# Optimization experiments

Hardware: AMD Instinct MI355X
Metric: run time of the kernel (lower is better)

## Reference

```python
import jax, jax.numpy as jnp
import numpy as np

DIM = 1024
H = 16
D = DIM // H
SCALE = D ** -0.5
EPS = 1e-5


def _layernorm(x, w, b):
    # force_fp32 LayerNorm over last axis
    xf = x.astype(jnp.float32)
    mu = xf.mean(-1, keepdims=True)
    var = xf.var(-1, keepdims=True)
    y = (xf - mu) / jnp.sqrt(var + EPS) * w.astype(jnp.float32) + b.astype(jnp.float32)
    return y.astype(x.dtype)


def setup_inputs() -> dict:
    key = jax.random.key(0)
    ks = jax.random.split(key, 8)
    x = jax.random.normal(ks[0], (2, 2048, DIM), dtype=jnp.float32)
    qkv_w = jax.random.normal(ks[1], (3 * DIM, DIM), dtype=jnp.float32) * (DIM ** -0.5)
    q_norm_w = jnp.ones((D,), jnp.float32)
    q_norm_b = jnp.zeros((D,), jnp.float32)
    k_norm_w = jnp.ones((D,), jnp.float32)
    k_norm_b = jnp.zeros((D,), jnp.float32)
    proj_w = jax.random.normal(ks[2], (DIM, DIM), dtype=jnp.float32) * (DIM ** -0.5)
    proj_b = jnp.zeros((DIM,), jnp.float32)
    return {"x": x, "qkv_w": qkv_w, "q_norm_w": q_norm_w, "q_norm_b": q_norm_b,
            "k_norm_w": k_norm_w, "k_norm_b": k_norm_b, "proj_w": proj_w, "proj_b": proj_b}


def reference(x, qkv_w, q_norm_w, q_norm_b, k_norm_w, k_norm_b, proj_w, proj_b):
    B, N, C = x.shape
    qkv = x @ qkv_w.T                                  # [B,N,3C]
    qkv = qkv.reshape(B, N, 3, H, D).transpose(2, 0, 3, 1, 4)  # [3,B,H,N,D]
    q, k, v = qkv[0], qkv[1], qkv[2]
    # per-head QK LayerNorm over head_dim
    q = _layernorm(q, q_norm_w, q_norm_b)
    k = _layernorm(k, k_norm_w, k_norm_b)
    # k-centering across sequence
    k = k - k.mean(-2, keepdims=True)
    attn = jnp.einsum('bhnd,bhmd->bhnm', q * SCALE, k)
    attn = attn - attn.max(-1, keepdims=True)
    attn = jax.nn.softmax(attn, axis=-1)
    out = jnp.einsum('bhnm,bhmd->bhnd', attn, v)       # [B,H,N,D]
    out = out.transpose(0, 2, 1, 3).reshape(B, N, C)
    return out @ proj_w.T + proj_b
```

## Files before the change

### kernel.cpp

```cpp
#include <hip/hip_runtime.h>
#include <cstdint>
#include <cstddef>

#define SEQ     2048
#define NBATCH  2
#define CDIM    1024
#define NHEAD   16
#define HDIM    64
#define MTOT    (NBATCH*SEQ)
#define C3      (3*CDIM)
#define LOG2E   1.44269504088896340736f
#define QKSCALE (0.125f*LOG2E)
#define LN_EPS  1e-5f

typedef unsigned short u16;
typedef short s16x8 __attribute__((ext_vector_type(8)));
typedef float f32x4  __attribute__((ext_vector_type(4)));
typedef float f32x16 __attribute__((ext_vector_type(16)));

static __device__ __forceinline__ f32x4 mfma16(s16x8 a, s16x8 b, f32x4 c) {
  return __builtin_amdgcn_mfma_f32_16x16x32_bf16(a, b, c, 0, 0, 0);
}
static __device__ __forceinline__ f32x16 mfma32(s16x8 a, s16x8 b, f32x16 c) {
  return __builtin_amdgcn_mfma_f32_32x32x16_bf16(a, b, c, 0, 0, 0);
}
static __device__ __forceinline__ float b2f(u16 v) {
  return __uint_as_float(((unsigned)v) << 16);
}
static __device__ __forceinline__ u16 f2b(float f) {
  unsigned u = __float_as_uint(f);
  u = u + 0x7fffu + ((u >> 16) & 1u);
  return (u16)(u >> 16);
}
static __device__ __forceinline__ float fexp2(float x) {
  float r;
  asm("v_exp_f32 %0, %1" : "=v"(r) : "v"(x));
  return r;
}

#define G2L16(g, l) __builtin_amdgcn_global_load_lds( \
    (__attribute__((address_space(1))) void*)(g),     \
    (__attribute__((address_space(3))) void*)(l), 16, 0, 0)

__global__ __launch_bounds__(256) void cast_f32_bf16(
    const float* __restrict__ in, u16* __restrict__ out, int n8)
{
  int i = blockIdx.x * 256 + threadIdx.x;
  if (i >= n8) return;
  float4 a = ((const float4*)in)[2*i];
  float4 b = ((const float4*)in)[2*i+1];
  union { u16 u[8]; uint4 v; } r;
  r.u[0]=f2b(a.x); r.u[1]=f2b(a.y); r.u[2]=f2b(a.z); r.u[3]=f2b(a.w);
  r.u[4]=f2b(b.x); r.u[5]=f2b(b.y); r.u[6]=f2b(b.z); r.u[7]=f2b(b.w);
  ((uint4*)out)[i] = r.v;
}

template<bool WRITE_BF16, bool BIAS>
__global__ __launch_bounds__(256) void gemm_nt(
    const u16* __restrict__ A, const u16* __restrict__ Bm,
    void* __restrict__ Cout, const float* __restrict__ bias,
    int M, int Nn, int K)
{
  __shared__ u16 As[128*64];
  __shared__ u16 Bs[128*64];
  const int tid = threadIdx.x;
  const int wave = tid >> 6, lane = tid & 63;
  const int l15 = lane & 15, l4 = lane >> 4;
  const int m0 = blockIdx.y * 128, n0 = blockIdx.x * 128;
  const int wr = (wave >> 1) * 64, wc = (wave & 1) * 64;
  f32x4 acc[4][4] = {};

  for (int k0 = 0; k0 < K; k0 += 64) {
    if (k0) __syncthreads();
#pragma unroll
    for (int i = 0; i < 4; ++i) {
      int ci  = (i*4 + wave)*64 + lane;
      int row = ci >> 3, ch = ci & 7;
      const u16* ga = A  + (size_t)(m0 + row)*K + k0 + ch*8;
      const u16* gb = Bm + (size_t)(n0 + row)*K + k0 + ch*8;
      G2L16(ga, As + (i*4 + wave)*512);
      G2L16(gb, Bs + (i*4 + wave)*512);
    }
    __syncthreads();

#pragma unroll
    for (int kk = 0; kk < 2; ++kk) {
      s16x8 af[4], bf[4];
#pragma unroll
      for (int r = 0; r < 4; ++r)
        af[r] = *(const s16x8*)(As + (wr + r*16 + l15)*64 + kk*32 + l4*8);
#pragma unroll
      for (int c = 0; c < 4; ++c)
        bf[c] = *(const s16x8*)(Bs + (wc + c*16 + l15)*64 + kk*32 + l4*8);
#pragma unroll
      for (int r = 0; r < 4; ++r)
#pragma unroll
        for (int c = 0; c < 4; ++c)
          acc[r][c] = mfma16(af[r], bf[c], acc[r][c]);
    }
  }

#pragma unroll
  for (int r = 0; r < 4; ++r)
#pragma unroll
    for (int c = 0; c < 4; ++c) {
      int row = m0 + wr + r*16 + l4*4;
      int col = n0 + wc + c*16 + l15;
#pragma unroll
      for (int q = 0; q < 4; ++q) {
        float v = acc[r][c][q];
        if (BIAS) v += bias[col];
        if (WRITE_BF16) ((u16*)Cout)[(size_t)(row + q)*Nn + col] = f2b(v);
        else           ((float*)Cout)[(size_t)(row + q)*Nn + col] = v;
      }
    }
}

__global__ __launch_bounds__(256) void ln_qk(
    const u16* __restrict__ qkv,
    const float* __restrict__ qw, const float* __restrict__ qb,
    const float* __restrict__ kw, const float* __restrict__ kb,
    u16* __restrict__ Qs, u16* __restrict__ Kn)
{
  int gw   = blockIdx.x * 4 + (threadIdx.x >> 6);
  int lane = threadIdx.x & 63;
  int m = gw >> 4, h = gw & 15;
  const u16* rowp = qkv + (size_t)m*C3 + h*HDIM + lane;
  int b = m >> 11, n = m & 2047;
  size_t o = ((size_t)(b*NHEAD + h)*SEQ + n)*HDIM + lane;

  float wq = qw[lane], bq = qb[lane], wk = kw[lane], bk = kb[lane];
  float xq = b2f(rowp[0]);
  float xk = b2f(rowp[CDIM]);
  float sq = xq, s2q = xq*xq, sk = xk, s2k = xk*xk;
#pragma unroll
  for (int off = 32; off; off >>= 1) {
    sq += __shfl_xor(sq, off, 64);  s2q += __shfl_xor(s2q, off, 64);
    sk += __shfl_xor(sk, off, 64);  s2k += __shfl_xor(s2k, off, 64);
  }
  float muq = sq*(1.f/64.f), varq = s2q*(1.f/64.f) - muq*muq;
  float muk = sk*(1.f/64.f), vark = s2k*(1.f/64.f) - muk*muk;
  float yq = (xq - muq) * (1.f/sqrtf(varq + LN_EPS)) * wq + bq;
  float yk = (xk - muk) * (1.f/sqrtf(vark + LN_EPS)) * wk + bk;
  Qs[o] = f2b(yq * QKSCALE);
  Kn[o] = f2b(yk);
}

__global__ __launch_bounds__(256) void v_transpose(
    const u16* __restrict__ qkv, u16* __restrict__ Vt)
{
  __shared__ u16 t[64][80];
  int bh = blockIdx.x, j0 = blockIdx.y * 64;
  int b = bh >> 4, h = bh & 15;
  int tid = threadIdx.x;
  int nl = tid >> 2, ch = tid & 3;
  const u16* src = qkv + (size_t)(b*SEQ + j0 + nl)*C3 + 2*CDIM + h*HDIM + ch*16;
  *(uint4*)&t[nl][ch*16]     = *(const uint4*)src;
  *(uint4*)&t[nl][ch*16 + 8] = *(const uint4*)(src + 8);
  __syncthreads();
  int d = tid >> 2, nc = tid & 3;
  u16 o[16];
#pragma unroll
  for (int i = 0; i < 16; ++i) o[i] = t[nc*16 + i][d];
  u16* dst = Vt + ((size_t)(bh*HDIM + d))*SEQ + j0 + nc*16;
  *(uint4*)dst       = *(uint4*)&o[0];
  *(uint4*)(dst + 8) = *(uint4*)&o[8];
}

__global__ __launch_bounds__(256) void flash_attn(
    const u16* __restrict__ Qs, const u16* __restrict__ Kn,
    const u16* __restrict__ Vt, u16* __restrict__ Oa)
{
  __shared__ u16 Kt[2][64*64];
  __shared__ u16 Vs[2][64*64];
  const int tid = threadIdx.x, wave = tid >> 6, lane = tid & 63;
  const int l31 = lane & 31, hi = lane >> 5;
  const int bh = blockIdx.y, q0 = blockIdx.x*128 + wave*32;
  const int sw = l31 & 7;

  const u16* Qrow = Qs + ((size_t)bh*SEQ + q0 + l31)*HDIM + hi*8;
  s16x8 qf[4];
#pragma unroll
  for (int ks = 0; ks < 4; ++ks)
    qf[ks] = *(const s16x8*)(Qrow + ks*16);

  f32x16 o0 = {}, o1 = {};
  float l_run = 0.f;

  const u16* Kg = Kn + (size_t)bh*SEQ*HDIM;
  const u16* Vg = Vt + (size_t)bh*HDIM*SEQ;

  auto STAGE = [&](int jb, int buf) {
#pragma unroll
    for (int i = 0; i < 2; ++i) {
      int ci = (i*4 + wave)*64 + lane;
      int row = ci >> 3, ch = ci & 7;
      int chs = ch ^ (row & 7);
      G2L16(Kg + (size_t)(jb + row)*HDIM + chs*8, Kt[buf] + (i*4 + wave)*512);
      G2L16(Vg + (size_t)row*SEQ + jb + chs*8,    Vs[buf] + (i*4 + wave)*512);
    }
  };

  STAGE(0, 0);
  __syncthreads();

  for (int t = 0; t < SEQ/64; ++t) {
    const int buf = t & 1;
    if (t + 1 < SEQ/64) STAGE((t+1)*64, buf ^ 1);
    const u16* Kb = Kt[buf];
    const u16* Vb = Vs[buf];

    f32x16 s0 = {}, s1 = {};
#pragma unroll
    for (int ks = 0; ks < 4; ++ks) {
      int ch = ((ks*2 + hi) ^ sw) * 8;
      s16x8 k0 = *(const s16x8*)(Kb + l31*64 + ch);
      s16x8 k1 = *(const s16x8*)(Kb + (32 + l31)*64 + ch);
      s0 = mfma32(k0, qf[ks], s0);
      s1 = mfma32(k1, qf[ks], s1);
    }

    float p0[16], p1[16];
#pragma unroll
    for (int i = 0; i < 16; ++i) p0[i] = fexp2(s0[i]);
#pragma unroll
    for (int i = 0; i < 16; ++i) p1[i] = fexp2(s1[i]);
    float s8[8];
#pragma unroll
    for (int i = 0; i < 8; ++i) s8[i] = (p0[i] + p0[i+8]) + (p1[i] + p1[i+8]);
    l_run += ((s8[0]+s8[1]) + (s8[2]+s8[3])) + ((s8[4]+s8[5]) + (s8[6]+s8[7]));

    s16x8 pf[4];
#pragma unroll
    for (int f = 0; f < 2; ++f) {
      const float* pp = f ? p1 : p0;
      unsigned pk[4][2];
#pragma unroll
      for (int q = 0; q < 4; ++q)
#pragma unroll
        for (int i = 0; i < 2; ++i)
          asm("v_cvt_pk_bf16_f32 %0, %1, %2"
              : "=v"(pk[q][i]) : "v"(pp[4*q+2*i]), "v"(pp[4*q+2*i+1]));
#pragma unroll
      for (int kc = 0; kc < 2; ++kc) {
        union { unsigned u[4]; s16x8 v; } bfu;
#pragma unroll
        for (int i = 0; i < 2; ++i) {
          unsigned x = pk[2*kc][i], y = pk[2*kc+1][i];
          asm("v_permlane32_swap_b32 %0, %1" : "+v"(x), "+v"(y));
          bfu.u[i] = x; bfu.u[2+i] = y;
        }
        pf[2*f+kc] = bfu.v;
      }
    }

#pragma unroll
    for (int s = 0; s < 4; ++s) {
      int ch = ((s*2 + hi) ^ sw) * 8;
      s16x8 v0 = *(const s16x8*)(Vb + l31*64 + ch);
      s16x8 v1 = *(const s16x8*)(Vb + (32 + l31)*64 + ch);
      o0 = mfma32(v0, pf[s], o0);
      o1 = mfma32(v1, pf[s], o1);
    }
    __syncthreads();
  }

  float l_all = l_run + __shfl_xor(l_run, 32, 64);
  float inv = 1.f / l_all;
  int b = bh >> 4, h = bh & 15;
  u16* dst = Oa + ((size_t)(b*SEQ + q0 + l31))*CDIM + h*HDIM;
#pragma unroll
  for (int df = 0; df < 2; ++df)
#pragma unroll
    for (int q2 = 0; q2 < 4; ++q2) {
      float a0, a1, a2, a3;
      if (df) { a0=o1[4*q2]; a1=o1[4*q2+1]; a2=o1[4*q2+2]; a3=o1[4*q2+3]; }
      else    { a0=o0[4*q2]; a1=o0[4*q2+1]; a2=o0[4*q2+2]; a3=o0[4*q2+3]; }
      a0 *= inv; a1 *= inv; a2 *= inv; a3 *= inv;
      unsigned w0, w1;
      asm("v_cvt_pk_bf16_f32 %0, %1, %2" : "=v"(w0) : "v"(a0), "v"(a1));
      asm("v_cvt_pk_bf16_f32 %0, %1, %2" : "=v"(w1) : "v"(a2), "v"(a3));
      uint2 st; st.x = w0; st.y = w1;
      *(uint2*)(dst + df*32 + q2*8 + hi*4) = st;
    }
}

extern "C" void kernel_launch(void* const* d_in, const int* in_sizes, int n_in,
                              void* d_out, int out_size, void* d_ws, size_t ws_size,
                              hipStream_t stream)
{
  const float* x      = (const float*)d_in[0];
  const float* qkv_w  = (const float*)d_in[1];
  const float* qnw    = (const float*)d_in[2];
  const float* qnb    = (const float*)d_in[3];
  const float* knw    = (const float*)d_in[4];
  const float* knb    = (const float*)d_in[5];
  const float* proj_w = (const float*)d_in[6];
  const float* proj_b = (const float*)d_in[7];
  float* out = (float*)d_out;

  char* ws = (char*)d_ws;
  u16* xb    = (u16*)(ws);
  u16* wqkv  = (u16*)(ws + (8ull  << 20));
  u16* wproj = (u16*)(ws + (14ull << 20));
  u16* qkvb  = (u16*)(ws + (16ull << 20));
  u16* Qsb   = (u16*)(ws + (40ull << 20));
  u16* Knb   = (u16*)(ws + (48ull << 20));
  u16* Vtb   = (u16*)(ws + (56ull << 20));
  u16* Oab   = (u16*)(ws + (64ull << 20));

  cast_f32_bf16<<<(MTOT*CDIM/8)/256, 256, 0, stream>>>(x, xb, MTOT*CDIM/8);
  cast_f32_bf16<<<(C3*CDIM/8)/256,   256, 0, stream>>>(qkv_w, wqkv, C3*CDIM/8);
  cast_f32_bf16<<<(CDIM*CDIM/8)/256, 256, 0, stream>>>(proj_w, wproj, CDIM*CDIM/8);

  gemm_nt<true, false><<<dim3(C3/128, MTOT/128), 256, 0, stream>>>(
      xb, wqkv, qkvb, nullptr, MTOT, C3, CDIM);

  ln_qk<<<(MTOT*NHEAD)/4, 256, 0, stream>>>(qkvb, qnw, qnb, knw, knb, Qsb, Knb);
  v_transpose<<<dim3(NBATCH*NHEAD, SEQ/64), 256, 0, stream>>>(qkvb, Vtb);

  flash_attn<<<dim3(SEQ/128, NBATCH*NHEAD), 256, 0, stream>>>(Qsb, Knb, Vtb, Oab);

  gemm_nt<false, true><<<dim3(CDIM/128, MTOT/128), 256, 0, stream>>>(
      Oab, wproj, out, proj_b, MTOT, CDIM, CDIM);
}
```

Baseline: 224.7 us.

## Fuse QK layernorm into QKV GEMM epilogue, merge casts, triple-buffer attention

Merges the three cast kernels into one launch and fuses the per-head Q/K LayerNorm into the QKV GEMM epilogue, using cross-lane shuffles over the 16 lanes that hold a head's 64 columns. This removes the ln_qk kernel and its round trip of Q/K through memory. The flash attention loop moves to a 3-stage LDS ring with explicit vmcnt waits, a single barrier per iteration and s_setprio around the MFMA blocks, so loads overlap more with compute. In exchange, LDS use and GEMM epilogue register pressure go up, and the Q/K stores in the epilogue are scattered.

Result: no change. 223.8 us (-0.4%).

```diff
diff --git a/kernel.cpp b/kernel.cpp
--- a/kernel.cpp
+++ b/kernel.cpp
@@ -42,24 +42,35 @@
     (__attribute__((address_space(1))) void*)(g),     \
     (__attribute__((address_space(3))) void*)(l), 16, 0, 0)
 
-__global__ __launch_bounds__(256) void cast_f32_bf16(
-    const float* __restrict__ in, u16* __restrict__ out, int n8)
+#define XSEG   (MTOT*CDIM/8)
+#define W1SEG  (C3*CDIM/8)
+#define W2SEG  (CDIM*CDIM/8)
+__global__ __launch_bounds__(256) void cast_all(
+    const float* __restrict__ x, const float* __restrict__ w1,
+    const float* __restrict__ w2, u16* __restrict__ xb,
+    u16* __restrict__ wqkv, u16* __restrict__ wproj)
 {
   int i = blockIdx.x * 256 + threadIdx.x;
-  if (i >= n8) return;
-  float4 a = ((const float4*)in)[2*i];
-  float4 b = ((const float4*)in)[2*i+1];
+  const float* src; u16* dst; int off;
+  if (i < XSEG)              { src = x;  dst = xb;    off = i; }
+  else if (i < XSEG + W1SEG) { src = w1; dst = wqkv;  off = i - XSEG; }
+  else                       { src = w2; dst = wproj; off = i - XSEG - W1SEG; }
+  float4 a = ((const float4*)src)[2*off];
+  float4 b = ((const float4*)src)[2*off+1];
   union { u16 u[8]; uint4 v; } r;
   r.u[0]=f2b(a.x); r.u[1]=f2b(a.y); r.u[2]=f2b(a.z); r.u[3]=f2b(a.w);
   r.u[4]=f2b(b.x); r.u[5]=f2b(b.y); r.u[6]=f2b(b.z); r.u[7]=f2b(b.w);
-  ((uint4*)out)[i] = r.v;
-}
-
-template<bool WRITE_BF16, bool BIAS>
+  ((uint4*)dst)[off] = r.v;
+}
+
+template<int MODE>
 __global__ __launch_bounds__(256) void gemm_nt(
     const u16* __restrict__ A, const u16* __restrict__ Bm,
     void* __restrict__ Cout, const float* __restrict__ bias,
-    int M, int Nn, int K)
+    int M, int Nn, int K,
+    const float* __restrict__ qw, const float* __restrict__ qb,
+    const float* __restrict__ kw, const float* __restrict__ kb,
+    u16* __restrict__ Qs, u16* __restrict__ Kn)
 {
   __shared__ u16 As[128*64];
   __shared__ u16 Bs[128*64];
@@ -100,50 +111,71 @@
     }
   }
 
-#pragma unroll
-  for (int r = 0; r < 4; ++r)
-#pragma unroll
-    for (int c = 0; c < 4; ++c) {
-      int row = m0 + wr + r*16 + l4*4;
-      int col = n0 + wc + c*16 + l15;
-#pragma unroll
-      for (int q = 0; q < 4; ++q) {
-        float v = acc[r][c][q];
-        if (BIAS) v += bias[col];
-        if (WRITE_BF16) ((u16*)Cout)[(size_t)(row + q)*Nn + col] = f2b(v);
-        else           ((float*)Cout)[(size_t)(row + q)*Nn + col] = v;
+  if (MODE == 0) {
+#pragma unroll
+    for (int r = 0; r < 4; ++r)
+#pragma unroll
+      for (int c = 0; c < 4; ++c) {
+        int row = m0 + wr + r*16 + l4*4;
+        int col = n0 + wc + c*16 + l15;
+#pragma unroll
+        for (int q = 0; q < 4; ++q)
+          ((float*)Cout)[(size_t)(row + q)*Nn + col] = acc[r][c][q] + bias[col];
       }
-    }
-}
-
-__global__ __launch_bounds__(256) void ln_qk(
-    const u16* __restrict__ qkv,
-    const float* __restrict__ qw, const float* __restrict__ qb,
-    const float* __restrict__ kw, const float* __restrict__ kb,
-    u16* __restrict__ Qs, u16* __restrict__ Kn)
-{
-  int gw   = blockIdx.x * 4 + (threadIdx.x >> 6);
-  int lane = threadIdx.x & 63;
-  int m = gw >> 4, h = gw & 15;
-  const u16* rowp = qkv + (size_t)m*C3 + h*HDIM + lane;
-  int b = m >> 11, n = m & 2047;
-  size_t o = ((size_t)(b*NHEAD + h)*SEQ + n)*HDIM + lane;
-
-  float wq = qw[lane], bq = qb[lane], wk = kw[lane], bk = kb[lane];
-  float xq = b2f(rowp[0]);
-  float xk = b2f(rowp[CDIM]);
-  float sq = xq, s2q = xq*xq, sk = xk, s2k = xk*xk;
-#pragma unroll
-  for (int off = 32; off; off >>= 1) {
-    sq += __shfl_xor(sq, off, 64);  s2q += __shfl_xor(s2q, off, 64);
-    sk += __shfl_xor(sk, off, 64);  s2k += __shfl_xor(s2k, off, 64);
+  } else {
+    const int colbase = n0 + wc;
+    if (colbase >= 2*CDIM) {
+#pragma unroll
+      for (int r = 0; r < 4; ++r)
+#pragma unroll
+        for (int c = 0; c < 4; ++c) {
+          int row = m0 + wr + r*16 + l4*4;
+          int col = colbase + c*16 + l15;
+#pragma unroll
+          for (int q = 0; q < 4; ++q)
+            ((u16*)Cout)[(size_t)(row + q)*Nn + col] = f2b(acc[r][c][q]);
+        }
+    } else {
+      const bool isQ = colbase < CDIM;
+      const int cq = isQ ? colbase : colbase - CDIM;
+      const int h  = cq >> 6;
+      const float* wv = isQ ? qw : kw;
+      const float* bv = isQ ? qb : kb;
+      u16* dst = isQ ? Qs : Kn;
+      const float scale = isQ ? QKSCALE : 1.f;
+      float wl[4], bl[4];
+#pragma unroll
+      for (int c = 0; c < 4; ++c) { wl[c] = wv[c*16 + l15]; bl[c] = bv[c*16 + l15]; }
+#pragma unroll
+      for (int r = 0; r < 4; ++r) {
+        float mu[4], rs[4];
+#pragma unroll
+        for (int q = 0; q < 4; ++q) {
+          float s = acc[r][0][q] + acc[r][1][q] + acc[r][2][q] + acc[r][3][q];
+          float s2 = acc[r][0][q]*acc[r][0][q] + acc[r][1][q]*acc[r][1][q]
+                   + acc[r][2][q]*acc[r][2][q] + acc[r][3][q]*acc[r][3][q];
+#pragma unroll
+          for (int off = 1; off < 16; off <<= 1) {
+            s  += __shfl_xor(s,  off, 64);
+            s2 += __shfl_xor(s2, off, 64);
+          }
+          float m_ = s * (1.f/64.f);
+          mu[q] = m_;
+          rs[q] = rsqrtf(s2 * (1.f/64.f) - m_*m_ + LN_EPS);
+        }
+#pragma unroll
+        for (int c = 0; c < 4; ++c)
+#pragma unroll
+          for (int q = 0; q < 4; ++q) {
+            int mrow = m0 + wr + r*16 + l4*4 + q;
+            int b = mrow >> 11, ns = mrow & 2047;
+            float y = (acc[r][c][q] - mu[q]) * rs[q] * wl[c] + bl[c];
+            dst[((size_t)(b*NHEAD + h)*SEQ + ns)*HDIM + c*16 + l15] =
+                f2b(y * scale);
+          }
+      }
+    }
   }
-  float muq = sq*(1.f/64.f), varq = s2q*(1.f/64.f) - muq*muq;
-  float muk = sk*(1.f/64.f), vark = s2k*(1.f/64.f) - muk*muk;
-  float yq = (xq - muq) * (1.f/sqrtf(varq + LN_EPS)) * wq + bq;
-  float yk = (xk - muk) * (1.f/sqrtf(vark + LN_EPS)) * wk + bk;
-  Qs[o] = f2b(yq * QKSCALE);
-  Kn[o] = f2b(yk);
 }
 
 __global__ __launch_bounds__(256) void v_transpose(
@@ -171,8 +203,8 @@
     const u16* __restrict__ Qs, const u16* __restrict__ Kn,
     const u16* __restrict__ Vt, u16* __restrict__ Oa)
 {
-  __shared__ u16 Kt[2][64*64];
-  __shared__ u16 Vs[2][64*64];
+  __shared__ u16 Kt[3][64*64];
+  __shared__ u16 Vs[3][64*64];
   const int tid = threadIdx.x, wave = tid >> 6, lane = tid & 63;
   const int l31 = lane & 31, hi = lane >> 5;
   const int bh = blockIdx.y, q0 = blockIdx.x*128 + wave*32;
@@ -202,15 +234,21 @@
   };
 
   STAGE(0, 0);
-  __syncthreads();
-
-  for (int t = 0; t < SEQ/64; ++t) {
-    const int buf = t & 1;
-    if (t + 1 < SEQ/64) STAGE((t+1)*64, buf ^ 1);
-    const u16* Kb = Kt[buf];
-    const u16* Vb = Vs[buf];
+  STAGE(64, 1);
+
+  const int NT = SEQ/64;
+  for (int t = 0; t < NT; ++t) {
+    if (t + 1 < NT) asm volatile("s_waitcnt vmcnt(4)" ::: "memory");
+    else            asm volatile("s_waitcnt vmcnt(0)" ::: "memory");
+    __builtin_amdgcn_s_barrier();
+    __builtin_amdgcn_sched_barrier(0);
+    if (t + 2 < NT) STAGE((t+2)*64, (t+2)%3);
+
+    const u16* Kb = Kt[t%3];
+    const u16* Vb = Vs[t%3];
 
     f32x16 s0 = {}, s1 = {};
+    __builtin_amdgcn_s_setprio(1);
 #pragma unroll
     for (int ks = 0; ks < 4; ++ks) {
       int ch = ((ks*2 + hi) ^ sw) * 8;
@@ -219,6 +257,7 @@
       s0 = mfma32(k0, qf[ks], s0);
       s1 = mfma32(k1, qf[ks], s1);
     }
+    __builtin_amdgcn_s_setprio(0);
 
     float p0[16], p1[16];
 #pragma unroll
@@ -254,6 +293,7 @@
       }
     }
 
+    __builtin_amdgcn_s_setprio(1);
 #pragma unroll
     for (int s = 0; s < 4; ++s) {
       int ch = ((s*2 + hi) ^ sw) * 8;
@@ -262,7 +302,7 @@
       o0 = mfma32(v0, pf[s], o0);
       o1 = mfma32(v1, pf[s], o1);
     }
-    __syncthreads();
+    __builtin_amdgcn_s_setprio(0);
   }
 
   float l_all = l_run + __shfl_xor(l_run, 32, 64);
@@ -309,18 +349,18 @@
   u16* Vtb   = (u16*)(ws + (56ull << 20));
   u16* Oab   = (u16*)(ws + (64ull << 20));
 
-  cast_f32_bf16<<<(MTOT*CDIM/8)/256, 256, 0, stream>>>(x, xb, MTOT*CDIM/8);
-  cast_f32_bf16<<<(C3*CDIM/8)/256,   256, 0, stream>>>(qkv_w, wqkv, C3*CDIM/8);
-  cast_f32_bf16<<<(CDIM*CDIM/8)/256, 256, 0, stream>>>(proj_w, wproj, CDIM*CDIM/8);
-
-  gemm_nt<true, false><<<dim3(C3/128, MTOT/128), 256, 0, stream>>>(
-      xb, wqkv, qkvb, nullptr, MTOT, C3, CDIM);
-
-  ln_qk<<<(MTOT*NHEAD)/4, 256, 0, stream>>>(qkvb, qnw, qnb, knw, knb, Qsb, Knb);
+  cast_all<<<(XSEG + W1SEG + W2SEG)/256, 256, 0, stream>>>(
+      x, qkv_w, proj_w, xb, wqkv, wproj);
+
+  gemm_nt<1><<<dim3(C3/128, MTOT/128), 256, 0, stream>>>(
+      xb, wqkv, qkvb, nullptr, MTOT, C3, CDIM,
+      qnw, qnb, knw, knb, Qsb, Knb);
+
   v_transpose<<<dim3(NBATCH*NHEAD, SEQ/64), 256, 0, stream>>>(qkvb, Vtb);
 
   flash_attn<<<dim3(SEQ/128, NBATCH*NHEAD), 256, 0, stream>>>(Qsb, Knb, Vtb, Oab);
 
-  gemm_nt<false, true><<<dim3(CDIM/128, MTOT/128), 256, 0, stream>>>(
-      Oab, wproj, out, proj_b, MTOT, CDIM, CDIM);
-}
+  gemm_nt<0><<<dim3(CDIM/128, MTOT/128), 256, 0, stream>>>(
+      Oab, wproj, out, proj_b, MTOT, CDIM, CDIM,
+      nullptr, nullptr, nullptr, nullptr, nullptr, nullptr);
+}
```

## Fuse casts, swizzle GEMM LDS, remap blocks, pipeline flash attention with V in registers

Applied to the files above, without the earlier changes.

Merges the three fp32-to-bf16 cast launches into one kernel and adds an XOR swizzle to the GEMM LDS tiles to cut bank conflicts. Swaps the GEMM grid axes so the M dimension runs along blockIdx.x, and remaps flash-attention blocks across XCDs. Flash attention now keeps K in a triple-buffered LDS ring and loads V straight from global into registers one tile ahead, with raw barriers and setprio around the MFMA sections. This trades register pressure and hand-written waitcnt/barrier correctness for less LDS traffic and fewer launches.

New measurement: 232.2 us. 1.03x slower.

```diff
diff --git a/kernel.cpp b/kernel.cpp
--- a/kernel.cpp
+++ b/kernel.cpp
@@ -42,17 +42,25 @@
     (__attribute__((address_space(1))) void*)(g),     \
     (__attribute__((address_space(3))) void*)(l), 16, 0, 0)
 
-__global__ __launch_bounds__(256) void cast_f32_bf16(
-    const float* __restrict__ in, u16* __restrict__ out, int n8)
+#define XSEG   (MTOT*CDIM/8)
+#define W1SEG  (C3*CDIM/8)
+#define W2SEG  (CDIM*CDIM/8)
+__global__ __launch_bounds__(256) void cast_all(
+    const float* __restrict__ x, const float* __restrict__ w1,
+    const float* __restrict__ w2, u16* __restrict__ xb,
+    u16* __restrict__ wqkv, u16* __restrict__ wproj)
 {
   int i = blockIdx.x * 256 + threadIdx.x;
-  if (i >= n8) return;
-  float4 a = ((const float4*)in)[2*i];
-  float4 b = ((const float4*)in)[2*i+1];
+  const float* src; u16* dst; int off;
+  if (i < XSEG)              { src = x;  dst = xb;    off = i; }
+  else if (i < XSEG + W1SEG) { src = w1; dst = wqkv;  off = i - XSEG; }
+  else                       { src = w2; dst = wproj; off = i - XSEG - W1SEG; }
+  float4 a = ((const float4*)src)[2*off];
+  float4 b = ((const float4*)src)[2*off+1];
   union { u16 u[8]; uint4 v; } r;
   r.u[0]=f2b(a.x); r.u[1]=f2b(a.y); r.u[2]=f2b(a.z); r.u[3]=f2b(a.w);
   r.u[4]=f2b(b.x); r.u[5]=f2b(b.y); r.u[6]=f2b(b.z); r.u[7]=f2b(b.w);
-  ((uint4*)out)[i] = r.v;
+  ((uint4*)dst)[off] = r.v;
 }
 
 template<bool WRITE_BF16, bool BIAS>
@@ -66,7 +74,7 @@
   const int tid = threadIdx.x;
   const int wave = tid >> 6, lane = tid & 63;
   const int l15 = lane & 15, l4 = lane >> 4;
-  const int m0 = blockIdx.y * 128, n0 = blockIdx.x * 128;
+  const int m0 = blockIdx.x * 128, n0 = blockIdx.y * 128;
   const int wr = (wave >> 1) * 64, wc = (wave & 1) * 64;
   f32x4 acc[4][4] = {};
 
@@ -76,8 +84,9 @@
     for (int i = 0; i < 4; ++i) {
       int ci  = (i*4 + wave)*64 + lane;
       int row = ci >> 3, ch = ci & 7;
-      const u16* ga = A  + (size_t)(m0 + row)*K + k0 + ch*8;
-      const u16* gb = Bm + (size_t)(n0 + row)*K + k0 + ch*8;
+      int chs = ch ^ (row & 7);
+      const u16* ga = A  + (size_t)(m0 + row)*K + k0 + chs*8;
+      const u16* gb = Bm + (size_t)(n0 + row)*K + k0 + chs*8;
       G2L16(ga, As + (i*4 + wave)*512);
       G2L16(gb, Bs + (i*4 + wave)*512);
     }
@@ -87,11 +96,15 @@
     for (int kk = 0; kk < 2; ++kk) {
       s16x8 af[4], bf[4];
 #pragma unroll
-      for (int r = 0; r < 4; ++r)
-        af[r] = *(const s16x8*)(As + (wr + r*16 + l15)*64 + kk*32 + l4*8);
-#pragma unroll
-      for (int c = 0; c < 4; ++c)
-        bf[c] = *(const s16x8*)(Bs + (wc + c*16 + l15)*64 + kk*32 + l4*8);
+      for (int r = 0; r < 4; ++r) {
+        int row = wr + r*16 + l15;
+        af[r] = *(const s16x8*)(As + row*64 + (((kk*4 + l4) ^ (row & 7))*8));
+      }
+#pragma unroll
+      for (int c = 0; c < 4; ++c) {
+        int row = wc + c*16 + l15;
+        bf[c] = *(const s16x8*)(Bs + row*64 + (((kk*4 + l4) ^ (row & 7))*8));
+      }
 #pragma unroll
       for (int r = 0; r < 4; ++r)
 #pragma unroll
@@ -171,11 +184,13 @@
     const u16* __restrict__ Qs, const u16* __restrict__ Kn,
     const u16* __restrict__ Vt, u16* __restrict__ Oa)
 {
-  __shared__ u16 Kt[2][64*64];
-  __shared__ u16 Vs[2][64*64];
+  __shared__ u16 Kt[3][64*64];
   const int tid = threadIdx.x, wave = tid >> 6, lane = tid & 63;
   const int l31 = lane & 31, hi = lane >> 5;
-  const int bh = blockIdx.y, q0 = blockIdx.x*128 + wave*32;
+  const int bid0 = blockIdx.x + blockIdx.y*16;
+  const int nid  = (bid0 & 7)*64 + (bid0 >> 3);
+  const int bh   = nid >> 4;
+  const int q0   = (nid & 15)*128 + wave*32;
   const int sw = l31 & 7;
 
   const u16* Qrow = Qs + ((size_t)bh*SEQ + q0 + l31)*HDIM + hi*8;
@@ -190,27 +205,26 @@
   const u16* Kg = Kn + (size_t)bh*SEQ*HDIM;
   const u16* Vg = Vt + (size_t)bh*HDIM*SEQ;
 
-  auto STAGE = [&](int jb, int buf) {
+  auto STAGEK = [&](int jb, int buf) {
 #pragma unroll
     for (int i = 0; i < 2; ++i) {
       int ci = (i*4 + wave)*64 + lane;
       int row = ci >> 3, ch = ci & 7;
       int chs = ch ^ (row & 7);
       G2L16(Kg + (size_t)(jb + row)*HDIM + chs*8, Kt[buf] + (i*4 + wave)*512);
-      G2L16(Vg + (size_t)row*SEQ + jb + chs*8,    Vs[buf] + (i*4 + wave)*512);
     }
   };
-
-  STAGE(0, 0);
-  __syncthreads();
-
-  for (int t = 0; t < SEQ/64; ++t) {
-    const int buf = t & 1;
-    if (t + 1 < SEQ/64) STAGE((t+1)*64, buf ^ 1);
-    const u16* Kb = Kt[buf];
-    const u16* Vb = Vs[buf];
-
+  auto LOADV = [&](int jb, s16x8* vf) {
+#pragma unroll
+    for (int s = 0; s < 4; ++s) {
+      vf[s]   = *(const s16x8*)(Vg + (size_t)l31*SEQ      + jb + (s*2+hi)*8);
+      vf[4+s] = *(const s16x8*)(Vg + (size_t)(32+l31)*SEQ + jb + (s*2+hi)*8);
+    }
+  };
+
+  auto TILE = [&](const u16* Kb, const s16x8* vf) {
     f32x16 s0 = {}, s1 = {};
+    __builtin_amdgcn_s_setprio(1);
 #pragma unroll
     for (int ks = 0; ks < 4; ++ks) {
       int ch = ((ks*2 + hi) ^ sw) * 8;
@@ -219,6 +233,7 @@
       s0 = mfma32(k0, qf[ks], s0);
       s1 = mfma32(k1, qf[ks], s1);
     }
+    __builtin_amdgcn_s_setprio(0);
 
     float p0[16], p1[16];
 #pragma unroll
@@ -254,15 +269,33 @@
       }
     }
 
+    __builtin_amdgcn_s_setprio(1);
 #pragma unroll
     for (int s = 0; s < 4; ++s) {
-      int ch = ((s*2 + hi) ^ sw) * 8;
-      s16x8 v0 = *(const s16x8*)(Vb + l31*64 + ch);
-      s16x8 v1 = *(const s16x8*)(Vb + (32 + l31)*64 + ch);
-      o0 = mfma32(v0, pf[s], o0);
-      o1 = mfma32(v1, pf[s], o1);
-    }
-    __syncthreads();
+      o0 = mfma32(vf[s],   pf[s], o0);
+      o1 = mfma32(vf[4+s], pf[s], o1);
+    }
+    __builtin_amdgcn_s_setprio(0);
+  };
+
+  s16x8 vA[8], vB[8];
+  STAGEK(0, 0);
+  STAGEK(64, 1);
+  LOADV(0, vA);
+  asm volatile("s_waitcnt vmcnt(8)" ::: "memory");
+
+  const int NT = SEQ/64;
+  for (int t = 0; t < NT; t += 2) {
+    __builtin_amdgcn_s_barrier();
+    __builtin_amdgcn_sched_barrier(0);
+    if (t + 2 < NT) STAGEK((t+2)*64, (t+2)%3);
+    LOADV((t+1)*64, vB);
+    TILE(Kt[t%3], vA);
+    __builtin_amdgcn_s_barrier();
+    __builtin_amdgcn_sched_barrier(0);
+    if (t + 3 < NT) STAGEK((t+3)*64, (t+3)%3);
+    if (t + 2 < NT) LOADV((t+2)*64, vA);
+    TILE(Kt[(t+1)%3], vB);
   }
 
   float l_all = l_run + __shfl_xor(l_run, 32, 64);
@@ -309,11 +342,10 @@
   u16* Vtb   = (u16*)(ws + (56ull << 20));
   u16* Oab   = (u16*)(ws + (64ull << 20));
 
-  cast_f32_bf16<<<(MTOT*CDIM/8)/256, 256, 0, stream>>>(x, xb, MTOT*CDIM/8);
-  cast_f32_bf16<<<(C3*CDIM/8)/256,   256, 0, stream>>>(qkv_w, wqkv, C3*CDIM/8);
-  cast_f32_bf16<<<(CDIM*CDIM/8)/256, 256, 0, stream>>>(proj_w, wproj, CDIM*CDIM/8);
-
-  gemm_nt<true, false><<<dim3(C3/128, MTOT/128), 256, 0, stream>>>(
+  cast_all<<<(XSEG + W1SEG + W2SEG)/256, 256, 0, stream>>>(
+      x, qkv_w, proj_w, xb, wqkv, wproj);
+
+  gemm_nt<true, false><<<dim3(MTOT/128, C3/128), 256, 0, stream>>>(
       xb, wqkv, qkvb, nullptr, MTOT, C3, CDIM);
 
   ln_qk<<<(MTOT*NHEAD)/4, 256, 0, stream>>>(qkvb, qnw, qnb, knw, knb, Qsb, Knb);
@@ -321,6 +353,6 @@
 
   flash_attn<<<dim3(SEQ/128, NBATCH*NHEAD), 256, 0, stream>>>(Qsb, Knb, Vtb, Oab);
 
-  gemm_nt<false, true><<<dim3(CDIM/128, MTOT/128), 256, 0, stream>>>(
+  gemm_nt<false, true><<<dim3(MTOT/128, CDIM/128), 256, 0, stream>>>(
       Oab, wproj, out, proj_b, MTOT, CDIM, CDIM);
 }
```
